# Kernel optimization log

Hardware: AMD Instinct MI355X
Metric: run time of the kernel (lower is better)

The kernel has to match this reference:

```python
import math
import jax, jax.numpy as jnp
import numpy as np


def setup_inputs() -> dict:
    key = jax.random.key(0)
    k1, k2, k3 = jax.random.split(key, 3)
    B, CK, CV = 2, 64, 384
    T, H, W = 8, 30, 54
    N = T * H * W
    mk = jax.random.normal(k1, (B, CK, N), dtype=jnp.float32)
    qk = jax.random.normal(k2, (B, CK, H, W), dtype=jnp.float32)
    mv = jax.random.normal(k3, (B, CV, N), dtype=jnp.float32)
    return {"mk": mk, "qk": qk, "mv": mv, "topk": 20}


def _compute_affinity(mk, qk, topk):
    # mk: [B, CK, N] memory keys; qk: [B, CK, H, W] query keys
    B, CK, H, W = qk.shape
    M = H * W
    qk2 = qk.reshape(B, CK, M)                      # [B, CK, M]
    a_sq = jnp.sum(mk * mk, axis=1)[:, :, None]     # [B, N, 1]
    ab = jnp.einsum('bcn,bcm->bnm', mk, qk2)        # [B, N, M]
    affinity = (2.0 * ab - a_sq) / math.sqrt(CK)    # negative sq-distance / sqrt(CK)
    N = affinity.shape[1]
    k = min(topk, N)
    # top-k over the memory axis (dim 1): move it last for lax.top_k
    aff_t = jnp.swapaxes(affinity, 1, 2)            # [B, M, N]
    vals, idx = jax.lax.top_k(aff_t, k)             # [B, M, k]
    vals = jax.nn.softmax(vals, axis=-1)
    b_ix = jnp.arange(B)[:, None, None]
    m_ix = jnp.arange(M)[None, :, None]
    sparse = jnp.zeros_like(aff_t).at[b_ix, m_ix, idx].set(vals)  # scatter softmaxed top-k
    return jnp.swapaxes(sparse, 1, 2)               # [B, N, M]


def reference(mk, qk, mv, topk):
    affinity = _compute_affinity(mk, qk, topk)      # [B, N, M]
    mem = jnp.einsum('bcn,bnm->bcm', mv, affinity)  # propagate_feat: bmm(mv, affinity)
    return mem
```

## Files before the change

kernel.cpp:

```cpp
#include <hip/hip_runtime.h>
#include <math.h>
#include <float.h>
#include <limits.h>
#include <stdint.h>

namespace {

constexpr int B  = 2;
constexpr int CK = 64;
constexpr int N  = 12960;
constexpr int M  = 1620;
constexpr int CV = 384;
constexpr int K  = 20;

constexpr int SEGN  = 1024;
constexpr int NSEG  = (N + SEGN - 1) / SEGN;
constexpr int CAP   = 64;
constexpr int SLOTS = NSEG * CAP;
constexpr int JC    = (SLOTS + 255) / 256;

static_assert((CAP & (CAP - 1)) == 0, "CAP must be pow2 (slot>>6 indexing)");
static_assert(NSEG * SEGN >= N, "segments must cover N");

__device__ __forceinline__ uint32_t f2k(float x) {
  uint32_t u = __float_as_uint(x);
  return u ^ ((u & 0x80000000u) ? 0xFFFFFFFFu : 0x80000000u);
}
__device__ __forceinline__ float k2f(uint32_t k) {
  uint32_t u = (k & 0x80000000u) ? (k ^ 0x80000000u) : ~k;
  return __uint_as_float(u);
}
__device__ __forceinline__ uint32_t umax2(uint32_t a, uint32_t b) { return a > b ? a : b; }
__device__ __forceinline__ uint32_t umin2(uint32_t a, uint32_t b) { return a < b ? a : b; }

__global__ __launch_bounds__(256) void transpose_kernel(const float* __restrict__ mv,
                                                        float* __restrict__ mvT) {
  __shared__ float tile[64][65];
  int b = blockIdx.z;
  int n0 = blockIdx.x * 64;
  int c0 = blockIdx.y * 64;
  int tx = threadIdx.x & 63, ty = threadIdx.x >> 6;
  for (int r = ty; r < 64; r += 4) {
    int c = c0 + r, n = n0 + tx;
    tile[r][tx] = (n < N) ? mv[((size_t)b * CV + c) * N + n] : 0.f;
  }
  __syncthreads();
  for (int r = ty; r < 64; r += 4) {
    int n = n0 + r, c = c0 + tx;
    if (n < N) mvT[((size_t)b * N + n) * CV + c] = tile[tx][r];
  }
}

__global__ __launch_bounds__(256) void transpose_out_kernel(const float* __restrict__ outT,
                                                            float* __restrict__ out) {
  __shared__ float tile[64][65];
  int b = blockIdx.z;
  int m0 = blockIdx.x * 64;
  int c0 = blockIdx.y * 64;
  int tx = threadIdx.x & 63, ty = threadIdx.x >> 6;
  for (int r = ty; r < 64; r += 4) {
    int m = m0 + r;
    if (m < M) tile[r][tx] = outT[((size_t)b * M + m) * CV + c0 + tx];
  }
  __syncthreads();
  for (int r = ty; r < 64; r += 4) {
    int c = c0 + r, m = m0 + tx;
    if (m < M) out[((size_t)b * CV + c) * M + m] = tile[tx][r];
  }
}

__global__ __launch_bounds__(256) void asq_kernel(const float* __restrict__ mk,
                                                  float* __restrict__ asq) {
  int i = blockIdx.x * 256 + threadIdx.x;
  if (i >= B * N) return;
  int b = i / N, n = i - b * N;
  const float* p = mk + (size_t)b * CK * N + n;
  float s = 0.f;
#pragma unroll
  for (int c = 0; c < CK; ++c) {
    float v = p[(size_t)c * N];
    s += v * v;
  }
  asq[i] = s;
}

__global__ __launch_bounds__(256) void fused_kernel(const float* __restrict__ mk,
                                                    const float* __restrict__ qk,
                                                    const float* __restrict__ asq,
                                                    uint32_t* __restrict__ cnt,
                                                    uint2* __restrict__ pairs) {
  const int b = blockIdx.z;
  const int seg = blockIdx.x;
  const int mg0 = blockIdx.y * 16;
  const int t = threadIdx.x;
  const int l = t & 63, w = t >> 6;

  __shared__ float qs[CK][20];
  __shared__ uint32_t scnt[16];

  for (int i = t; i < CK * 16; i += 256) {
    int c = i >> 4, ml = i & 15;
    int m = mg0 + ml;
    qs[c][ml] = (m < M) ? qk[((size_t)b * CK + c) * M + m] : 0.f;
  }
  if (t < 16) scnt[t] = 0u;
  __syncthreads();

  const int nb = seg * SEGN + 4 * l;
  bool vch[4];
#pragma unroll
  for (int ch = 0; ch < 4; ++ch) vch[ch] = (nb + ch * 256) < N;

  const float* mkb = mk + (size_t)b * CK * N + nb;

  float4 acc[4][4];
#pragma unroll
  for (int mj = 0; mj < 4; ++mj)
#pragma unroll
    for (int ch = 0; ch < 4; ++ch) acc[mj][ch] = make_float4(0.f, 0.f, 0.f, 0.f);

#pragma unroll 2
  for (int c = 0; c < CK; ++c) {
    float4 kv[4];
#pragma unroll
    for (int ch = 0; ch < 4; ++ch)
      kv[ch] = vch[ch] ? *reinterpret_cast<const float4*>(mkb + (size_t)c * N + ch * 256)
                       : make_float4(0.f, 0.f, 0.f, 0.f);
    const float4 qv = *reinterpret_cast<const float4*>(&qs[c][w * 4]);
    const float qm[4] = {qv.x, qv.y, qv.z, qv.w};
#pragma unroll
    for (int mj = 0; mj < 4; ++mj)
#pragma unroll
      for (int ch = 0; ch < 4; ++ch) {
        acc[mj][ch].x += kv[ch].x * qm[mj];
        acc[mj][ch].y += kv[ch].y * qm[mj];
        acc[mj][ch].z += kv[ch].z * qm[mj];
        acc[mj][ch].w += kv[ch].w * qm[mj];
      }
  }

  float4 sq[4];
#pragma unroll
  for (int ch = 0; ch < 4; ++ch)
    sq[ch] = vch[ch] ? *reinterpret_cast<const float4*>(asq + (size_t)b * N + nb + ch * 256)
                     : make_float4(0.f, 0.f, 0.f, 0.f);

  for (int mj = 0; mj < 4; ++mj) {
    const int m = mg0 + w * 4 + mj;
    if (m >= M) break;
    uint32_t key[16];
    uint32_t lmax = 0u;
#pragma unroll
    for (int ch = 0; ch < 4; ++ch) {
      const float vx = (2.f * acc[mj][ch].x - sq[ch].x) * 0.125f;
      const float vy = (2.f * acc[mj][ch].y - sq[ch].y) * 0.125f;
      const float vz = (2.f * acc[mj][ch].z - sq[ch].z) * 0.125f;
      const float vw = (2.f * acc[mj][ch].w - sq[ch].w) * 0.125f;
      key[ch * 4 + 0] = vch[ch] ? f2k(vx) : 0u;
      key[ch * 4 + 1] = vch[ch] ? f2k(vy) : 0u;
      key[ch * 4 + 2] = vch[ch] ? f2k(vz) : 0u;
      key[ch * 4 + 3] = vch[ch] ? f2k(vw) : 0u;
      lmax = umax2(lmax, umax2(umax2(key[ch * 4 + 0], key[ch * 4 + 1]),
                               umax2(key[ch * 4 + 2], key[ch * 4 + 3])));
    }
    uint32_t s = lmax;
#pragma unroll
    for (int kk = 2; kk <= 64; kk <<= 1) {
#pragma unroll
      for (int jj = kk >> 1; jj > 0; jj >>= 1) {
        uint32_t o = __shfl_xor(s, jj, 64);
        bool keepMin = (((l & kk) == 0) == ((l & jj) == 0));
        s = keepMin ? umin2(s, o) : umax2(s, o);
      }
    }
    const uint32_t theta = __shfl(s, 44, 64);
    const size_t base = ((size_t)(b * M + m) * NSEG + seg) * CAP;
#pragma unroll
    for (int r = 0; r < 16; ++r) {
      if (key[r] >= theta) {
        uint32_t slot = atomicAdd(&scnt[w * 4 + mj], 1u);
        if (slot < CAP)
          pairs[base + slot] = make_uint2(key[r], (uint32_t)(nb + (r >> 2) * 256 + (r & 3)));
      }
    }
  }
  if (l < 4) {
    const int m = mg0 + w * 4 + l;
    if (m < M) {
      uint32_t c0 = scnt[w * 4 + l];
      cnt[(size_t)(b * M + m) * NSEG + seg] = (c0 < CAP) ? c0 : (uint32_t)CAP;
    }
  }
}

__global__ __launch_bounds__(256) void merge_topk_gather(const uint32_t* __restrict__ cnt,
                                                         const uint2* __restrict__ pairs,
                                                         const float* __restrict__ mvT,
                                                         float* __restrict__ outT) {
  const int m = blockIdx.x, b = blockIdx.y;
  const int t = threadIdx.x;

  __shared__ uint32_t segc[NSEG];
  constexpr int HP = 268;
  __shared__ int hist[4][4][HP];
  __shared__ int s_digit, s_before;
  __shared__ int wn[K];
  __shared__ uint32_t wk[K];
  __shared__ float sw[K];
  __shared__ int gcnt, ecnt, s_last;
  __shared__ int ebuf[K];
  __shared__ int rmin4[4];

  if (t < NSEG) segc[t] = cnt[(size_t)(b * M + m) * NSEG + t];
  __syncthreads();

  const uint2* pb = pairs + (size_t)(b * M + m) * SLOTS;
  uint32_t k[JC];
  uint32_t nn[JC];
#pragma unroll
  for (int j = 0; j < JC; ++j) {
    int idx = t + (j << 8);
    bool valid = (idx < SLOTS) && ((uint32_t)(idx & (CAP - 1)) < segc[idx >> 6]);
    if (valid) {
      uint2 pr = pb[idx];
      k[j] = pr.x;
      nn[j] = pr.y;
    } else {
      k[j] = 0u;
      nn[j] = 0u;
    }
  }

  int before = 0;
  uint32_t pref = 0;
  const int w = t >> 6;
  const int rp = (t >> 4) & 3;
  int* myhist = &hist[w][rp][0];

  for (int p = 0; p < 4; ++p) {
    const int s = 24 - 8 * p;
    for (int i = t; i < 16 * HP; i += 256) ((int*)hist)[i] = 0;
    __syncthreads();
    const int shHi = (p == 0) ? 0 : (s + 8);
#pragma unroll
    for (int j = 0; j < JC; ++j) {
      uint32_t key = k[j];
      bool act = (p == 0) || ((key >> shHi) == pref);
      if (act) atomicAdd(&myhist[(key >> s) & 255], 1);
    }
    __syncthreads();
    if (t < 64) {
      int d = 4 * t;
      int4 g = make_int4(0, 0, 0, 0);
#pragma unroll
      for (int ww = 0; ww < 4; ++ww)
#pragma unroll
        for (int rr = 0; rr < 4; ++rr) {
          int4 h = *reinterpret_cast<int4*>(&hist[ww][rr][d]);
          g.x += h.x; g.y += h.y; g.z += h.z; g.w += h.w;
        }
      int sl = g.x + g.y + g.z + g.w;
      int sfx = sl;
#pragma unroll
      for (int off = 1; off < 64; off <<= 1) {
        int o = __shfl_down(sfx, off);
        sfx += (t + off < 64) ? o : 0;
      }
      int above = sfx - sl;
      int rem = K - before;
      if (above < rem && rem <= sfx) {
        int cum = above, ds;
        if (cum + g.w >= rem) ds = 3;
        else { cum += g.w;
          if (cum + g.z >= rem) ds = 2;
          else { cum += g.z;
            if (cum + g.y >= rem) ds = 1;
            else { cum += g.y; ds = 0; } } }
        s_digit = 4 * t + ds;
        s_before = before + cum;
      }
    }
    __syncthreads();
    pref = (pref << 8) | (uint32_t)s_digit;
    before = s_before;
  }

  const uint32_t thr = pref;
  const int need = K - before;
  if (t == 0) { gcnt = 0; ecnt = 0; }
  __syncthreads();
#pragma unroll
  for (int j = 0; j < JC; ++j) {
    uint32_t key = k[j];
    if (key > thr) {
      int q = atomicAdd(&gcnt, 1);
      wn[q] = (int)nn[j]; wk[q] = key;
    } else if (key == thr) {
      int q = atomicAdd(&ecnt, 1);
      if (q < K) ebuf[q] = (int)nn[j];
    }
  }
  __syncthreads();
  if (ecnt == need) {
    if (t < need) { wn[before + t] = ebuf[t]; wk[before + t] = thr; }
  } else {
    int last = -1;
    for (int r = 0; r < need; ++r) {
      int loc = INT_MAX;
#pragma unroll
      for (int j = 0; j < JC; ++j) {
        int n = (int)nn[j];
        if (k[j] == thr && n > last && n < loc) loc = n;
      }
#pragma unroll
      for (int off = 1; off < 64; off <<= 1) loc = min(loc, __shfl_xor(loc, off));
      if ((t & 63) == 0) rmin4[t >> 6] = loc;
      __syncthreads();
      if (t == 0) {
        int mn = min(min(rmin4[0], rmin4[1]), min(rmin4[2], rmin4[3]));
        wn[before + r] = mn; wk[before + r] = thr; s_last = mn;
      }
      __syncthreads();
      last = s_last;
    }
  }
  __syncthreads();

  if (t < 64) {
    float v = (t < K) ? k2f(wk[t]) : -FLT_MAX;
    float mx = v;
#pragma unroll
    for (int off = 1; off < 64; off <<= 1) mx = fmaxf(mx, __shfl_xor(mx, off));
    float e = (t < K) ? expf(v - mx) : 0.f;
    float ss = e;
#pragma unroll
    for (int off = 1; off < 64; off <<= 1) ss += __shfl_xor(ss, off);
    if (t < K) sw[t] = e / ss;
  }
  __syncthreads();

  if (t < CV / 4) {
    const float4* tb4 = reinterpret_cast<const float4*>(mvT + (size_t)b * N * CV);
    float4 s4 = make_float4(0.f, 0.f, 0.f, 0.f);
#pragma unroll
    for (int j = 0; j < K; ++j) {
      float wj = sw[j];
      float4 v = tb4[(size_t)wn[j] * (CV / 4) + t];
      s4.x += wj * v.x; s4.y += wj * v.y; s4.z += wj * v.z; s4.w += wj * v.w;
    }
    reinterpret_cast<float4*>(outT + ((size_t)b * M + m) * CV)[t] = s4;
  }
}

}

extern "C" void kernel_launch(void* const* d_in, const int* in_sizes, int n_in,
                              void* d_out, int out_size, void* d_ws, size_t ws_size,
                              hipStream_t stream) {
  const float* mk = (const float*)d_in[0];
  const float* qk = (const float*)d_in[1];
  const float* mv = (const float*)d_in[2];
  float* out = (float*)d_out;

  char* w = (char*)d_ws;
  float* asq = (float*)w;
  size_t o = (size_t)B * N * sizeof(float);
  float* mvT = (float*)(w + o);
  o += (size_t)B * N * CV * sizeof(float);
  float* outT = (float*)(w + o);
  o += (size_t)B * M * CV * sizeof(float);
  uint32_t* cnt = (uint32_t*)(w + o);
  o += (size_t)B * M * NSEG * sizeof(uint32_t);
  uint2* pairs = (uint2*)(w + o);
  o += (size_t)B * M * NSEG * CAP * sizeof(uint2);

  transpose_kernel<<<dim3((N + 63) / 64, CV / 64, B), 256, 0, stream>>>(mv, mvT);
  asq_kernel<<<(B * N + 255) / 256, 256, 0, stream>>>(mk, asq);
  fused_kernel<<<dim3(NSEG, (M + 15) / 16, B), 256, 0, stream>>>(mk, qk, asq, cnt, pairs);
  merge_topk_gather<<<dim3(M, B), 256, 0, stream>>>(cnt, pairs, mvT, outT);
  transpose_out_kernel<<<dim3((M + 63) / 64, CV / 64, B), 256, 0, stream>>>(outT, out);
}
```

Baseline: 251.3 us.

## Split fused kernel into full/tail variants, ballot compaction, interleaved bitonic selects

The fused distance+candidate kernel becomes a template with a FULL variant that skips bounds checks for all complete segments, plus a separate tail launch for the last partial segment. Shared-memory atomic slot allocation is replaced with wave-level ballot/popcount compaction. The four per-row bitonic threshold sorts now run interleaved on floats, which adds instruction-level parallelism. The costs are an extra kernel launch and more live registers from holding all 64 scores at once.

```diff
diff --git a/kernel.cpp b/kernel.cpp
--- a/kernel.cpp
+++ b/kernel.cpp
@@ -30,8 +30,6 @@
   uint32_t u = (k & 0x80000000u) ? (k ^ 0x80000000u) : ~k;
   return __uint_as_float(u);
 }
-__device__ __forceinline__ uint32_t umax2(uint32_t a, uint32_t b) { return a > b ? a : b; }
-__device__ __forceinline__ uint32_t umin2(uint32_t a, uint32_t b) { return a < b ? a : b; }
 
 __global__ __launch_bounds__(256) void transpose_kernel(const float* __restrict__ mv,
                                                         float* __restrict__ mvT) {
@@ -84,34 +82,34 @@
   asq[i] = s;
 }
 
+template <bool FULL>
 __global__ __launch_bounds__(256) void fused_kernel(const float* __restrict__ mk,
                                                     const float* __restrict__ qk,
                                                     const float* __restrict__ asq,
                                                     uint32_t* __restrict__ cnt,
-                                                    uint2* __restrict__ pairs) {
+                                                    uint2* __restrict__ pairs,
+                                                    int seg0) {
   const int b = blockIdx.z;
-  const int seg = blockIdx.x;
+  const int seg = seg0 + blockIdx.x;
   const int mg0 = blockIdx.y * 16;
   const int t = threadIdx.x;
   const int l = t & 63, w = t >> 6;
 
   __shared__ float qs[CK][20];
-  __shared__ uint32_t scnt[16];
 
   for (int i = t; i < CK * 16; i += 256) {
     int c = i >> 4, ml = i & 15;
     int m = mg0 + ml;
     qs[c][ml] = (m < M) ? qk[((size_t)b * CK + c) * M + m] : 0.f;
   }
-  if (t < 16) scnt[t] = 0u;
   __syncthreads();
 
   const int nb = seg * SEGN + 4 * l;
   bool vch[4];
 #pragma unroll
-  for (int ch = 0; ch < 4; ++ch) vch[ch] = (nb + ch * 256) < N;
-
-  const float* mkb = mk + (size_t)b * CK * N + nb;
+  for (int ch = 0; ch < 4; ++ch) vch[ch] = FULL || ((nb + ch * 256) < N);
+
+  const float* p = mk + (size_t)b * CK * N + nb;
 
   float4 acc[4][4];
 #pragma unroll
@@ -122,10 +120,17 @@
 #pragma unroll 2
   for (int c = 0; c < CK; ++c) {
     float4 kv[4];
-#pragma unroll
-    for (int ch = 0; ch < 4; ++ch)
-      kv[ch] = vch[ch] ? *reinterpret_cast<const float4*>(mkb + (size_t)c * N + ch * 256)
-                       : make_float4(0.f, 0.f, 0.f, 0.f);
+    if (FULL) {
+      kv[0] = *reinterpret_cast<const float4*>(p);
+      kv[1] = *reinterpret_cast<const float4*>(p + 256);
+      kv[2] = *reinterpret_cast<const float4*>(p + 512);
+      kv[3] = *reinterpret_cast<const float4*>(p + 768);
+    } else {
+#pragma unroll
+      for (int ch = 0; ch < 4; ++ch)
+        kv[ch] = vch[ch] ? *reinterpret_cast<const float4*>(p + ch * 256)
+                         : make_float4(0.f, 0.f, 0.f, 0.f);
+    }
     const float4 qv = *reinterpret_cast<const float4*>(&qs[c][w * 4]);
     const float qm[4] = {qv.x, qv.y, qv.z, qv.w};
 #pragma unroll
@@ -137,6 +142,7 @@
         acc[mj][ch].z += kv[ch].z * qm[mj];
         acc[mj][ch].w += kv[ch].w * qm[mj];
       }
+    p += N;
   }
 
   float4 sq[4];
@@ -145,51 +151,71 @@
     sq[ch] = vch[ch] ? *reinterpret_cast<const float4*>(asq + (size_t)b * N + nb + ch * 256)
                      : make_float4(0.f, 0.f, 0.f, 0.f);
 
+  float v[4][16];
+#pragma unroll
+  for (int mj = 0; mj < 4; ++mj)
+#pragma unroll
+    for (int ch = 0; ch < 4; ++ch) {
+      const float rx = (2.f * acc[mj][ch].x - sq[ch].x) * 0.125f;
+      const float ry = (2.f * acc[mj][ch].y - sq[ch].y) * 0.125f;
+      const float rz = (2.f * acc[mj][ch].z - sq[ch].z) * 0.125f;
+      const float rw = (2.f * acc[mj][ch].w - sq[ch].w) * 0.125f;
+      v[mj][ch * 4 + 0] = (FULL || vch[ch]) ? rx : -FLT_MAX;
+      v[mj][ch * 4 + 1] = (FULL || vch[ch]) ? ry : -FLT_MAX;
+      v[mj][ch * 4 + 2] = (FULL || vch[ch]) ? rz : -FLT_MAX;
+      v[mj][ch * 4 + 3] = (FULL || vch[ch]) ? rw : -FLT_MAX;
+    }
+
+  float lm[4];
+#pragma unroll
+  for (int mj = 0; mj < 4; ++mj) {
+    float a = fmaxf(fmaxf(v[mj][0], v[mj][1]), fmaxf(v[mj][2], v[mj][3]));
+    float bb = fmaxf(fmaxf(v[mj][4], v[mj][5]), fmaxf(v[mj][6], v[mj][7]));
+    float c2 = fmaxf(fmaxf(v[mj][8], v[mj][9]), fmaxf(v[mj][10], v[mj][11]));
+    float d = fmaxf(fmaxf(v[mj][12], v[mj][13]), fmaxf(v[mj][14], v[mj][15]));
+    lm[mj] = fmaxf(fmaxf(a, bb), fmaxf(c2, d));
+  }
+
+  float s0 = lm[0], s1 = lm[1], s2 = lm[2], s3 = lm[3];
+#pragma unroll
+  for (int kk = 2; kk <= 64; kk <<= 1) {
+#pragma unroll
+    for (int jj = kk >> 1; jj > 0; jj >>= 1) {
+      const float o0 = __shfl_xor(s0, jj, 64);
+      const float o1 = __shfl_xor(s1, jj, 64);
+      const float o2 = __shfl_xor(s2, jj, 64);
+      const float o3 = __shfl_xor(s3, jj, 64);
+      const bool keepMin = (((l & kk) == 0) == ((l & jj) == 0));
+      s0 = keepMin ? fminf(s0, o0) : fmaxf(s0, o0);
+      s1 = keepMin ? fminf(s1, o1) : fmaxf(s1, o1);
+      s2 = keepMin ? fminf(s2, o2) : fmaxf(s2, o2);
+      s3 = keepMin ? fminf(s3, o3) : fmaxf(s3, o3);
+    }
+  }
+  const float th[4] = {__shfl(s0, 44, 64), __shfl(s1, 44, 64),
+                       __shfl(s2, 44, 64), __shfl(s3, 44, 64)};
+
+  const uint64_t lmlt = (1ull << l) - 1ull;
   for (int mj = 0; mj < 4; ++mj) {
     const int m = mg0 + w * 4 + mj;
     if (m >= M) break;
-    uint32_t key[16];
-    uint32_t lmax = 0u;
-#pragma unroll
-    for (int ch = 0; ch < 4; ++ch) {
-      const float vx = (2.f * acc[mj][ch].x - sq[ch].x) * 0.125f;
-      const float vy = (2.f * acc[mj][ch].y - sq[ch].y) * 0.125f;
-      const float vz = (2.f * acc[mj][ch].z - sq[ch].z) * 0.125f;
-      const float vw = (2.f * acc[mj][ch].w - sq[ch].w) * 0.125f;
-      key[ch * 4 + 0] = vch[ch] ? f2k(vx) : 0u;
-      key[ch * 4 + 1] = vch[ch] ? f2k(vy) : 0u;
-      key[ch * 4 + 2] = vch[ch] ? f2k(vz) : 0u;
-      key[ch * 4 + 3] = vch[ch] ? f2k(vw) : 0u;
-      lmax = umax2(lmax, umax2(umax2(key[ch * 4 + 0], key[ch * 4 + 1]),
-                               umax2(key[ch * 4 + 2], key[ch * 4 + 3])));
-    }
-    uint32_t s = lmax;
-#pragma unroll
-    for (int kk = 2; kk <= 64; kk <<= 1) {
-#pragma unroll
-      for (int jj = kk >> 1; jj > 0; jj >>= 1) {
-        uint32_t o = __shfl_xor(s, jj, 64);
-        bool keepMin = (((l & kk) == 0) == ((l & jj) == 0));
-        s = keepMin ? umin2(s, o) : umax2(s, o);
-      }
-    }
-    const uint32_t theta = __shfl(s, 44, 64);
-    const size_t base = ((size_t)(b * M + m) * NSEG + seg) * CAP;
+    const size_t pbase = ((size_t)(b * M + m) * NSEG + seg) * CAP;
+    const float thf = th[mj];
+    int base = 0;
 #pragma unroll
     for (int r = 0; r < 16; ++r) {
-      if (key[r] >= theta) {
-        uint32_t slot = atomicAdd(&scnt[w * 4 + mj], 1u);
-        if (slot < CAP)
-          pairs[base + slot] = make_uint2(key[r], (uint32_t)(nb + (r >> 2) * 256 + (r & 3)));
-      }
-    }
-  }
-  if (l < 4) {
-    const int m = mg0 + w * 4 + l;
-    if (m < M) {
-      uint32_t c0 = scnt[w * 4 + l];
-      cnt[(size_t)(b * M + m) * NSEG + seg] = (c0 < CAP) ? c0 : (uint32_t)CAP;
-    }
+      const bool hit = v[mj][r] >= thf;
+      const uint64_t mask = __ballot(hit);
+      if (hit) {
+        const int pos = base + (int)__popcll(mask & lmlt);
+        if (pos < CAP)
+          pairs[pbase + pos] =
+              make_uint2(f2k(v[mj][r]), (uint32_t)(nb + (r >> 2) * 256 + (r & 3)));
+      }
+      base += (int)__popcll(mask);
+    }
+    if (l == 0)
+      cnt[(size_t)(b * M + m) * NSEG + seg] = (uint32_t)(base < CAP ? base : CAP);
   }
 }
 
@@ -345,8 +371,8 @@
 #pragma unroll
     for (int j = 0; j < K; ++j) {
       float wj = sw[j];
-      float4 v = tb4[(size_t)wn[j] * (CV / 4) + t];
-      s4.x += wj * v.x; s4.y += wj * v.y; s4.z += wj * v.z; s4.w += wj * v.w;
+      float4 vv = tb4[(size_t)wn[j] * (CV / 4) + t];
+      s4.x += wj * vv.x; s4.y += wj * vv.y; s4.z += wj * vv.z; s4.w += wj * vv.w;
     }
     reinterpret_cast<float4*>(outT + ((size_t)b * M + m) * CV)[t] = s4;
   }
@@ -376,7 +402,9 @@
 
   transpose_kernel<<<dim3((N + 63) / 64, CV / 64, B), 256, 0, stream>>>(mv, mvT);
   asq_kernel<<<(B * N + 255) / 256, 256, 0, stream>>>(mk, asq);
-  fused_kernel<<<dim3(NSEG, (M + 15) / 16, B), 256, 0, stream>>>(mk, qk, asq, cnt, pairs);
+  const int MG = (M + 15) / 16;
+  fused_kernel<true><<<dim3(NSEG - 1, MG, B), 256, 0, stream>>>(mk, qk, asq, cnt, pairs, 0);
+  fused_kernel<false><<<dim3(1, MG, B), 256, 0, stream>>>(mk, qk, asq, cnt, pairs, NSEG - 1);
   merge_topk_gather<<<dim3(M, B), 256, 0, stream>>>(cnt, pairs, mvT, outT);
   transpose_out_kernel<<<dim3((M + 63) / 64, CV / 64, B), 256, 0, stream>>>(outT, out);
 }
```

After: 267.0 us. +6.3%, slower.

## Restructure fused distance kernel: per-wave N chunks, LDS transpose, ballot compaction

Applied to the files above, without the earlier changes.

The fused score kernel now gives each wave its own 256-wide chunk of the memory axis and all 16 query columns, instead of 4 query columns over the whole 1024-wide segment. Each mk load therefore feeds 16 queries rather than 4, cutting global key loads per FMA. Scores are staged through a 16 KB LDS buffer so each wave can still run the per-query threshold selection over the full segment. Atomic slot allocation is replaced with ballot/popcount compaction, the mk loads are software-pipelined two channels ahead, and a template removes bounds checks for full segments. The cost is extra LDS traffic and block-wide syncs in the selection phase, plus higher register use for 16 float4 accumulators.

```diff
diff --git a/kernel.cpp b/kernel.cpp
--- a/kernel.cpp
+++ b/kernel.cpp
@@ -30,8 +30,6 @@
   uint32_t u = (k & 0x80000000u) ? (k ^ 0x80000000u) : ~k;
   return __uint_as_float(u);
 }
-__device__ __forceinline__ uint32_t umax2(uint32_t a, uint32_t b) { return a > b ? a : b; }
-__device__ __forceinline__ uint32_t umin2(uint32_t a, uint32_t b) { return a < b ? a : b; }
 
 __global__ __launch_bounds__(256) void transpose_kernel(const float* __restrict__ mv,
                                                         float* __restrict__ mvT) {
@@ -84,113 +82,148 @@
   asq[i] = s;
 }
 
+template <bool FULL>
+__device__ __forceinline__ void fused_body(const float* __restrict__ mk,
+                                           const float* __restrict__ qk,
+                                           const float* __restrict__ asq,
+                                           uint32_t* __restrict__ cnt,
+                                           uint2* __restrict__ pairs,
+                                           float (&qs)[CK][20],
+                                           float (&vv)[4][SEGN]) {
+  const int b = blockIdx.z;
+  const int seg = blockIdx.x;
+  const int mg0 = blockIdx.y * 16;
+  const int t = threadIdx.x;
+  const int l = t & 63, w = t >> 6;
+
+  for (int i = t; i < CK * 16; i += 256) {
+    int c = i >> 4, ml = i & 15;
+    int m = mg0 + ml;
+    qs[c][ml] = (m < M) ? qk[((size_t)b * CK + c) * M + m] : 0.f;
+  }
+  __syncthreads();
+
+  const int nl0 = w * 256 + 4 * l;
+  const int nb  = seg * SEGN + nl0;
+  const bool vld = FULL || (nb < N);
+
+  const float* p = mk + (size_t)b * CK * N + nb;
+
+  float4 acc[16];
+#pragma unroll
+  for (int m = 0; m < 16; ++m) acc[m] = make_float4(0.f, 0.f, 0.f, 0.f);
+
+  auto ld = [&](const float* q) -> float4 {
+    return vld ? *reinterpret_cast<const float4*>(q) : make_float4(0.f, 0.f, 0.f, 0.f);
+  };
+  auto fmastep = [&](const float4& kv, int c) {
+    const float4 q0 = *reinterpret_cast<const float4*>(&qs[c][0]);
+    const float4 q1 = *reinterpret_cast<const float4*>(&qs[c][4]);
+    const float4 q2 = *reinterpret_cast<const float4*>(&qs[c][8]);
+    const float4 q3 = *reinterpret_cast<const float4*>(&qs[c][12]);
+    const float qm[16] = {q0.x, q0.y, q0.z, q0.w, q1.x, q1.y, q1.z, q1.w,
+                          q2.x, q2.y, q2.z, q2.w, q3.x, q3.y, q3.z, q3.w};
+#pragma unroll
+    for (int m = 0; m < 16; ++m) {
+      acc[m].x += kv.x * qm[m];
+      acc[m].y += kv.y * qm[m];
+      acc[m].z += kv.z * qm[m];
+      acc[m].w += kv.w * qm[m];
+    }
+  };
+
+  float4 kva = ld(p);
+  float4 kvb = ld(p + N);
+  const float* pn = p + 2 * (size_t)N;
+#pragma unroll 2
+  for (int c = 0; c < CK - 2; ++c) {
+    const float4 kvn = ld(pn);
+    pn += N;
+    fmastep(kva, c);
+    kva = kvb;
+    kvb = kvn;
+  }
+  fmastep(kva, CK - 2);
+  fmastep(kvb, CK - 1);
+
+  float4 sq4 = make_float4(0.f, 0.f, 0.f, 0.f);
+  if (vld) sq4 = *reinterpret_cast<const float4*>(asq + (size_t)b * N + nb);
+
+  const uint64_t lmlt = (1ull << l) - 1ull;
+
+#pragma unroll 1
+  for (int r = 0; r < 4; ++r) {
+#pragma unroll
+    for (int mj = 0; mj < 4; ++mj) {
+      const float4 a = acc[4 * r + mj];
+      float4 vr;
+      vr.x = (2.f * a.x - sq4.x) * 0.125f;
+      vr.y = (2.f * a.y - sq4.y) * 0.125f;
+      vr.z = (2.f * a.z - sq4.z) * 0.125f;
+      vr.w = (2.f * a.w - sq4.w) * 0.125f;
+      if (!FULL && !vld) vr = make_float4(-FLT_MAX, -FLT_MAX, -FLT_MAX, -FLT_MAX);
+      *reinterpret_cast<float4*>(&vv[mj][nl0]) = vr;
+    }
+    __syncthreads();
+    const int m = mg0 + 4 * r + w;
+    if (m < M) {
+      float vloc[16];
+#pragma unroll
+      for (int j = 0; j < 4; ++j) {
+        const float4 q = *reinterpret_cast<const float4*>(&vv[w][4 * l + 256 * j]);
+        vloc[4 * j + 0] = q.x;
+        vloc[4 * j + 1] = q.y;
+        vloc[4 * j + 2] = q.z;
+        vloc[4 * j + 3] = q.w;
+      }
+      float a0 = fmaxf(fmaxf(vloc[0], vloc[1]), fmaxf(vloc[2], vloc[3]));
+      float a1 = fmaxf(fmaxf(vloc[4], vloc[5]), fmaxf(vloc[6], vloc[7]));
+      float a2 = fmaxf(fmaxf(vloc[8], vloc[9]), fmaxf(vloc[10], vloc[11]));
+      float a3 = fmaxf(fmaxf(vloc[12], vloc[13]), fmaxf(vloc[14], vloc[15]));
+      float s = fmaxf(fmaxf(a0, a1), fmaxf(a2, a3));
+#pragma unroll
+      for (int kk = 2; kk <= 64; kk <<= 1) {
+#pragma unroll
+        for (int jj = kk >> 1; jj > 0; jj >>= 1) {
+          const float o = __shfl_xor(s, jj, 64);
+          const bool keepMin = (((l & kk) == 0) == ((l & jj) == 0));
+          s = keepMin ? fminf(s, o) : fmaxf(s, o);
+        }
+      }
+      const float th = __shfl(s, 44, 64);
+      const size_t pbase = ((size_t)(b * M + m) * NSEG + seg) * CAP;
+      int base = 0;
+#pragma unroll
+      for (int r16 = 0; r16 < 16; ++r16) {
+        const bool hit = vloc[r16] >= th;
+        const uint64_t mask = __ballot(hit);
+        if (hit) {
+          const int pos = base + (int)__popcll(mask & lmlt);
+          if (pos < CAP)
+            pairs[pbase + pos] = make_uint2(
+                f2k(vloc[r16]),
+                (uint32_t)(seg * SEGN + 4 * l + 256 * (r16 >> 2) + (r16 & 3)));
+        }
+        base += (int)__popcll(mask);
+      }
+      if (l == 0)
+        cnt[(size_t)(b * M + m) * NSEG + seg] = (uint32_t)(base < CAP ? base : CAP);
+    }
+    __syncthreads();
+  }
+}
+
 __global__ __launch_bounds__(256) void fused_kernel(const float* __restrict__ mk,
                                                     const float* __restrict__ qk,
                                                     const float* __restrict__ asq,
                                                     uint32_t* __restrict__ cnt,
                                                     uint2* __restrict__ pairs) {
-  const int b = blockIdx.z;
-  const int seg = blockIdx.x;
-  const int mg0 = blockIdx.y * 16;
-  const int t = threadIdx.x;
-  const int l = t & 63, w = t >> 6;
-
   __shared__ float qs[CK][20];
-  __shared__ uint32_t scnt[16];
-
-  for (int i = t; i < CK * 16; i += 256) {
-    int c = i >> 4, ml = i & 15;
-    int m = mg0 + ml;
-    qs[c][ml] = (m < M) ? qk[((size_t)b * CK + c) * M + m] : 0.f;
-  }
-  if (t < 16) scnt[t] = 0u;
-  __syncthreads();
-
-  const int nb = seg * SEGN + 4 * l;
-  bool vch[4];
-#pragma unroll
-  for (int ch = 0; ch < 4; ++ch) vch[ch] = (nb + ch * 256) < N;
-
-  const float* mkb = mk + (size_t)b * CK * N + nb;
-
-  float4 acc[4][4];
-#pragma unroll
-  for (int mj = 0; mj < 4; ++mj)
-#pragma unroll
-    for (int ch = 0; ch < 4; ++ch) acc[mj][ch] = make_float4(0.f, 0.f, 0.f, 0.f);
-
-#pragma unroll 2
-  for (int c = 0; c < CK; ++c) {
-    float4 kv[4];
-#pragma unroll
-    for (int ch = 0; ch < 4; ++ch)
-      kv[ch] = vch[ch] ? *reinterpret_cast<const float4*>(mkb + (size_t)c * N + ch * 256)
-                       : make_float4(0.f, 0.f, 0.f, 0.f);
-    const float4 qv = *reinterpret_cast<const float4*>(&qs[c][w * 4]);
-    const float qm[4] = {qv.x, qv.y, qv.z, qv.w};
-#pragma unroll
-    for (int mj = 0; mj < 4; ++mj)
-#pragma unroll
-      for (int ch = 0; ch < 4; ++ch) {
-        acc[mj][ch].x += kv[ch].x * qm[mj];
-        acc[mj][ch].y += kv[ch].y * qm[mj];
-        acc[mj][ch].z += kv[ch].z * qm[mj];
-        acc[mj][ch].w += kv[ch].w * qm[mj];
-      }
-  }
-
-  float4 sq[4];
-#pragma unroll
-  for (int ch = 0; ch < 4; ++ch)
-    sq[ch] = vch[ch] ? *reinterpret_cast<const float4*>(asq + (size_t)b * N + nb + ch * 256)
-                     : make_float4(0.f, 0.f, 0.f, 0.f);
-
-  for (int mj = 0; mj < 4; ++mj) {
-    const int m = mg0 + w * 4 + mj;
-    if (m >= M) break;
-    uint32_t key[16];
-    uint32_t lmax = 0u;
-#pragma unroll
-    for (int ch = 0; ch < 4; ++ch) {
-      const float vx = (2.f * acc[mj][ch].x - sq[ch].x) * 0.125f;
-      const float vy = (2.f * acc[mj][ch].y - sq[ch].y) * 0.125f;
-      const float vz = (2.f * acc[mj][ch].z - sq[ch].z) * 0.125f;
-      const float vw = (2.f * acc[mj][ch].w - sq[ch].w) * 0.125f;
-      key[ch * 4 + 0] = vch[ch] ? f2k(vx) : 0u;
-      key[ch * 4 + 1] = vch[ch] ? f2k(vy) : 0u;
-      key[ch * 4 + 2] = vch[ch] ? f2k(vz) : 0u;
-      key[ch * 4 + 3] = vch[ch] ? f2k(vw) : 0u;
-      lmax = umax2(lmax, umax2(umax2(key[ch * 4 + 0], key[ch * 4 + 1]),
-                               umax2(key[ch * 4 + 2], key[ch * 4 + 3])));
-    }
-    uint32_t s = lmax;
-#pragma unroll
-    for (int kk = 2; kk <= 64; kk <<= 1) {
-#pragma unroll
-      for (int jj = kk >> 1; jj > 0; jj >>= 1) {
-        uint32_t o = __shfl_xor(s, jj, 64);
-        bool keepMin = (((l & kk) == 0) == ((l & jj) == 0));
-        s = keepMin ? umin2(s, o) : umax2(s, o);
-      }
-    }
-    const uint32_t theta = __shfl(s, 44, 64);
-    const size_t base = ((size_t)(b * M + m) * NSEG + seg) * CAP;
-#pragma unroll
-    for (int r = 0; r < 16; ++r) {
-      if (key[r] >= theta) {
-        uint32_t slot = atomicAdd(&scnt[w * 4 + mj], 1u);
-        if (slot < CAP)
-          pairs[base + slot] = make_uint2(key[r], (uint32_t)(nb + (r >> 2) * 256 + (r & 3)));
-      }
-    }
-  }
-  if (l < 4) {
-    const int m = mg0 + w * 4 + l;
-    if (m < M) {
-      uint32_t c0 = scnt[w * 4 + l];
-      cnt[(size_t)(b * M + m) * NSEG + seg] = (c0 < CAP) ? c0 : (uint32_t)CAP;
-    }
-  }
+  __shared__ float vv[4][SEGN];
+  if (blockIdx.x != NSEG - 1)
+    fused_body<true>(mk, qk, asq, cnt, pairs, qs, vv);
+  else
+    fused_body<false>(mk, qk, asq, cnt, pairs, qs, vv);
 }
 
 __global__ __launch_bounds__(256) void merge_topk_gather(const uint32_t* __restrict__ cnt,
@@ -345,8 +378,8 @@
 #pragma unroll
     for (int j = 0; j < K; ++j) {
       float wj = sw[j];
-      float4 v = tb4[(size_t)wn[j] * (CV / 4) + t];
-      s4.x += wj * v.x; s4.y += wj * v.y; s4.z += wj * v.z; s4.w += wj * v.w;
+      float4 vv4 = tb4[(size_t)wn[j] * (CV / 4) + t];
+      s4.x += wj * vv4.x; s4.y += wj * vv4.y; s4.z += wj * vv4.z; s4.w += wj * vv4.w;
     }
     reinterpret_cast<float4*>(outT + ((size_t)b * M + m) * CV)[t] = s4;
   }
@@ -376,7 +409,8 @@
 
   transpose_kernel<<<dim3((N + 63) / 64, CV / 64, B), 256, 0, stream>>>(mv, mvT);
   asq_kernel<<<(B * N + 255) / 256, 256, 0, stream>>>(mk, asq);
-  fused_kernel<<<dim3(NSEG, (M + 15) / 16, B), 256, 0, stream>>>(mk, qk, asq, cnt, pairs);
+  const int MG = (M + 15) / 16;
+  fused_kernel<<<dim3(NSEG, MG, B), 256, 0, stream>>>(mk, qk, asq, cnt, pairs);
   merge_topk_gather<<<dim3(M, B), 256, 0, stream>>>(cnt, pairs, mvT, outT);
   transpose_out_kernel<<<dim3((M + 63) / 64, CV / 64, B), 256, 0, stream>>>(outT, out);
 }
```

After: 295.7 us. 1.18x slower.
